# Optimization experiments

Hardware: AMD Instinct MI355X
Metric: run time of the kernel (lower is better)

The kernel has to match this reference:

```python
import jax, jax.numpy as jnp
import numpy as np

RBF_DIM = 64          # args.radius_emb_dim
FOLD_DIM = 128        # args.fold_dim
PROT_RADIUS = 30.0    # args.protein_radius (GaussianSmearing stop)
NP_, NL_, E_ = 100000, 50000, 500000


def gaussian_smearing(d):
    # GaussianSmearing(start=0, stop=PROT_RADIUS, num_gaussians=RBF_DIM)
    offsets = jnp.linspace(0.0, PROT_RADIUS, RBF_DIM, dtype=d.dtype)  # [R]
    coeff = -0.5 / (offsets[1] - offsets[0]) ** 2
    return jnp.exp(coeff * (d[:, None] - offsets[None, :]) ** 2)  # [E, R]


def setup_inputs() -> dict:
    key = jax.random.key(0)
    ks = jax.random.split(key, 12)
    scale = 10.0  # spread positions so distances span [0, PROT_RADIUS]
    pos = lambda k, n: jax.random.normal(k, (n, 3), jnp.float32) * scale
    inp = {
        'lig_pos': pos(ks[0], NL_),
        'prot_pos': pos(ks[1], NP_),
        'prot_pos_Cb': pos(ks[2], NP_),
        'prot_pos_C': pos(ks[3], NP_),
        'prot_pos_O': pos(ks[4], NP_),
        'prot_pos_N': pos(ks[5], NP_),
        'W1': jax.random.normal(ks[6], (5 * RBF_DIM, FOLD_DIM), jnp.float32) * 0.05,
        'b1': jnp.zeros((FOLD_DIM,), jnp.float32),
        'W2': jax.random.normal(ks[7], (FOLD_DIM, FOLD_DIM), jnp.float32) * 0.05,
        'b2': jnp.zeros((FOLD_DIM,), jnp.float32),
        'src': jax.random.randint(ks[8], (E_,), 0, NL_, jnp.int32),   # ligand index per edge
        'dst': jax.random.randint(ks[9], (E_,), 0, NP_, jnp.int32),   # protein index per edge
    }
    return inp


def reference(lig_pos, prot_pos, prot_pos_Cb, prot_pos_C, prot_pos_O, prot_pos_N,
              W1, b1, W2, b2, src, dst):
    lp = lig_pos[src]  # [E, 3] gather of ligand positions
    # 5 distance channels: CA/Cb/C/O/N protein atoms, each RBF-smeared
    feats = [gaussian_smearing(jnp.linalg.norm(lp - p[dst], axis=-1))
             for p in (prot_pos, prot_pos_Cb, prot_pos_C, prot_pos_O, prot_pos_N)]
    edge_attr = jnp.concatenate(feats, axis=-1)  # [E, 5*RBF_DIM]
    h = jax.nn.relu(edge_attr @ W1 + b1)         # [E, FOLD_DIM]
    return h @ W2 + b2                           # [E, FOLD_DIM]
```

## Files before the change

### kernel.cpp

```cpp
#include <hip/hip_runtime.h>
#include <hip/hip_bf16.h>

typedef unsigned short ushort_t;
typedef unsigned int uint_t;
typedef __attribute__((ext_vector_type(8))) short short8;
typedef __attribute__((ext_vector_type(4))) float f32x4;
typedef __attribute__((ext_vector_type(4))) uint_t uint4_t;
typedef __attribute__((ext_vector_type(2))) uint_t uint2_t;

#define FOLD 128
#define S_CONST 1.78357580f
#define DS_CONST 0.84932180f

__device__ __forceinline__ ushort_t f2bf(float f) {
    uint_t x = __builtin_bit_cast(uint_t, f);
    x += 0x7FFFu + ((x >> 16) & 1u);
    return (ushort_t)(x >> 16);
}

__device__ __forceinline__ uint_t pkbf(float a, float b) {
    uint_t xl = __builtin_bit_cast(uint_t, a);
    uint_t xh = __builtin_bit_cast(uint_t, b);
    uint_t rl = (xl + 0x7FFFu + ((xl >> 16) & 1u)) >> 16;
    uint_t rh = (xh + 0x7FFFu + ((xh >> 16) & 1u)) & 0xFFFF0000u;
    return rh | rl;
}

__global__ __launch_bounds__(256) void pack_w(const float* __restrict__ W1,
                                              const float* __restrict__ W2,
                                              ushort_t* __restrict__ W1p,
                                              ushort_t* __restrict__ W2p) {
    int i = blockIdx.x * 256 + threadIdx.x;
    if (i < 40960) {
        int j = i & 7, l = (i >> 3) & 63, nt = (i >> 9) & 7, ks = i >> 12;
        int row = ks * 32 + ((l >> 4) << 3) + j;
        int col = nt * 16 + (l & 15);
        W1p[i] = f2bf(W1[row * FOLD + col]);
    } else if (i < 40960 + 16384) {
        int q = i - 40960;
        int j = q & 7, l = (q >> 3) & 63, nt = (q >> 9) & 7, ks = q >> 12;
        int row = ks * 32 + ((l >> 4) << 3) + j;
        int col = nt * 16 + (l & 15);
        W2p[q] = f2bf(W2[row * FOLD + col]);
    }
}

#define TEDGE 64

__global__ __launch_bounds__(256, 2) void fused(
    const float* __restrict__ lig,
    const float* __restrict__ p0, const float* __restrict__ p1,
    const float* __restrict__ p2, const float* __restrict__ p3,
    const float* __restrict__ p4,
    const ushort_t* __restrict__ W1p, const ushort_t* __restrict__ W2p,
    const float* __restrict__ b1, const float* __restrict__ b2,
    const int* __restrict__ src, const int* __restrict__ dst,
    float* __restrict__ out, int E)
{
    __shared__ float d_lds[2][5][TEDGE];
    __shared__ alignas(16) uint_t attrU[TEDGE * 160];
    __shared__ alignas(16) uint_t h_u[TEDGE * 64];

    const int t = threadIdx.x;
    const int w = t >> 6;
    const int l = t & 63;
    const int lrow = l & 15, lgrp = l >> 4;
    const int aswz = (lrow & 7) << 2;
    const int ntiles = (E + TEDGE - 1) / TEDGE;

    const short8* W1v = reinterpret_cast<const short8*>(W1p);
    const short8* W2v = reinterpret_cast<const short8*>(W2p);
    short8 wb1[20], wb2[8];
    #pragma unroll
    for (int ks = 0; ks < 10; ++ks) {
        wb1[2 * ks]     = W1v[(ks * 8 + w * 2 + 0) * 64 + l];
        wb1[2 * ks + 1] = W1v[(ks * 8 + w * 2 + 1) * 64 + l];
    }
    #pragma unroll
    for (int ks = 0; ks < 4; ++ks) {
        wb2[2 * ks]     = W2v[(ks * 8 + w * 2 + 0) * 64 + l];
        wb2[2 * ks + 1] = W2v[(ks * 8 + w * 2 + 1) * 64 + l];
    }
    f32x4 hb1[2], hb2[2];
    hb1[0] = *reinterpret_cast<const f32x4*>(&b1[w * 32 + lgrp * 4]);
    hb1[1] = *reinterpret_cast<const f32x4*>(&b1[w * 32 + 16 + lgrp * 4]);
    hb2[0] = *reinterpret_cast<const f32x4*>(&b2[w * 32 + lgrp * 4]);
    hb2[1] = *reinterpret_cast<const f32x4*>(&b2[w * 32 + 16 + lgrp * 4]);

    const int g1c = t >> 6, g1m = t & 63;
    const bool gth2 = (t < 64);
    const float* GP1 = (g1c == 0) ? p0 : (g1c == 1) ? p1 : (g1c == 2) ? p2 : p3;
    const float* GP2 = p4;

    const int m2 = t >> 3, q2 = t & 7;
    const float ubase = (float)(8 * q2) * DS_CONST;

    int tile = blockIdx.x;
    if (tile >= ntiles) return;

    {
        int e = tile * TEDGE + g1m; if (e >= E) e = E - 1;
        int s = src[e], dd = dst[e];
        float dx = lig[3 * s]     - GP1[3 * dd];
        float dy = lig[3 * s + 1] - GP1[3 * dd + 1];
        float dz = lig[3 * s + 2] - GP1[3 * dd + 2];
        d_lds[0][g1c][g1m] = sqrtf(dx * dx + dy * dy + dz * dz);
        if (gth2) {
            float ex = lig[3 * s]     - GP2[3 * dd];
            float ey = lig[3 * s + 1] - GP2[3 * dd + 1];
            float ez = lig[3 * s + 2] - GP2[3 * dd + 2];
            d_lds[0][4][g1m] = sqrtf(ex * ex + ey * ey + ez * ez);
        }
    }
    __syncthreads();

    int buf = 0;
    while (true) {
        const int next = tile + gridDim.x;
        const bool havenext = (next < ntiles);

        float ax, ay, az, bx, by, bz, cx, cy, cz;
        if (havenext) {
            int e = next * TEDGE + g1m; if (e >= E) e = E - 1;
            int s = src[e], dd = dst[e];
            ax = lig[3 * s];     bx = GP1[3 * dd];
            ay = lig[3 * s + 1]; by = GP1[3 * dd + 1];
            az = lig[3 * s + 2]; bz = GP1[3 * dd + 2];
            if (gth2) {
                cx = GP2[3 * dd]; cy = GP2[3 * dd + 1]; cz = GP2[3 * dd + 2];
            }
        }

        #pragma unroll
        for (int half = 0; half < 2; ++half) {
            const int m = m2 + half * 32;
            const int swz = (m & 7) << 2;
            float dv[5];
            #pragma unroll
            for (int c = 0; c < 5; ++c) dv[c] = d_lds[buf][c][m];
            #pragma unroll
            for (int c = 0; c < 5; ++c) {
                float u0 = __builtin_fmaf(dv[c], S_CONST, -ubase);
                uint4_t vals;
                #pragma unroll
                for (int i = 0; i < 4; ++i) {
                    float ua = u0 - (float)(2 * i) * DS_CONST;
                    float ub = u0 - (float)(2 * i + 1) * DS_CONST;
                    float va = __builtin_amdgcn_exp2f(-(ua * ua));
                    float vb = __builtin_amdgcn_exp2f(-(ub * ub));
                    vals[i] = pkbf(va, vb);
                }
                int o = 32 * c + 4 * q2;
                *reinterpret_cast<uint4_t*>(&attrU[m * 160 + (o ^ swz)]) = vals;
            }
        }

        if (havenext) {
            float dx = ax - bx, dy = ay - by, dz = az - bz;
            d_lds[buf ^ 1][g1c][g1m] = sqrtf(dx * dx + dy * dy + dz * dz);
            if (gth2) {
                float ex = ax - cx, ey = ay - cy, ez = az - cz;
                d_lds[buf ^ 1][4][g1m] = sqrtf(ex * ex + ey * ey + ez * ez);
            }
        }
        __syncthreads();

        f32x4 g1[2][4];
        #pragma unroll
        for (int nh = 0; nh < 2; ++nh)
            #pragma unroll
            for (int eh = 0; eh < 4; ++eh) g1[nh][eh] = f32x4{0.f, 0.f, 0.f, 0.f};
        #pragma unroll
        for (int ks = 0; ks < 10; ++ks) {
            int o = ks * 16 + lgrp * 4;
            short8 af[4];
            #pragma unroll
            for (int eh = 0; eh < 4; ++eh)
                af[eh] = *reinterpret_cast<const short8*>(&attrU[(lrow + eh * 16) * 160 + (o ^ aswz)]);
            #pragma unroll
            for (int eh = 0; eh < 4; ++eh) {
                g1[0][eh] = __builtin_amdgcn_mfma_f32_16x16x32_bf16(wb1[2 * ks],     af[eh], g1[0][eh], 0, 0, 0);
                g1[1][eh] = __builtin_amdgcn_mfma_f32_16x16x32_bf16(wb1[2 * ks + 1], af[eh], g1[1][eh], 0, 0, 0);
            }
        }

        #pragma unroll
        for (int nh = 0; nh < 2; ++nh) {
            #pragma unroll
            for (int eh = 0; eh < 4; ++eh) {
                float v0 = fmaxf(g1[nh][eh][0] + hb1[nh][0], 0.f);
                float v1 = fmaxf(g1[nh][eh][1] + hb1[nh][1], 0.f);
                float v2 = fmaxf(g1[nh][eh][2] + hb1[nh][2], 0.f);
                float v3 = fmaxf(g1[nh][eh][3] + hb1[nh][3], 0.f);
                uint2_t pv;
                pv[0] = pkbf(v0, v1);
                pv[1] = pkbf(v2, v3);
                int e = eh * 16 + lrow;
                int dw = (w * 16 + nh * 8 + lgrp * 2) ^ ((e & 7) << 2);
                *reinterpret_cast<uint2_t*>(&h_u[e * 64 + dw]) = pv;
            }
        }
        __syncthreads();

        f32x4 o2[2][4];
        #pragma unroll
        for (int nh = 0; nh < 2; ++nh)
            #pragma unroll
            for (int eh = 0; eh < 4; ++eh) o2[nh][eh] = f32x4{0.f, 0.f, 0.f, 0.f};
        #pragma unroll
        for (int ks = 0; ks < 4; ++ks) {
            int dw = ks * 16 + lgrp * 4;
            short8 hf[4];
            #pragma unroll
            for (int eh = 0; eh < 4; ++eh)
                hf[eh] = *reinterpret_cast<const short8*>(&h_u[(lrow + eh * 16) * 64 + (dw ^ aswz)]);
            #pragma unroll
            for (int eh = 0; eh < 4; ++eh) {
                o2[0][eh] = __builtin_amdgcn_mfma_f32_16x16x32_bf16(wb2[2 * ks],     hf[eh], o2[0][eh], 0, 0, 0);
                o2[1][eh] = __builtin_amdgcn_mfma_f32_16x16x32_bf16(wb2[2 * ks + 1], hf[eh], o2[1][eh], 0, 0, 0);
            }
        }

        const int e0i = tile * TEDGE;
        #pragma unroll
        for (int nh = 0; nh < 2; ++nh) {
            #pragma unroll
            for (int eh = 0; eh < 4; ++eh) {
                int e = e0i + eh * 16 + lrow;
                if (e < E) {
                    f32x4 v = o2[nh][eh] + hb2[nh];
                    *reinterpret_cast<f32x4*>(&out[(size_t)e * FOLD + w * 32 + nh * 16 + lgrp * 4]) = v;
                }
            }
        }

        if (!havenext) break;
        tile = next;
        buf ^= 1;
    }
}

extern "C" void kernel_launch(void* const* d_in, const int* in_sizes, int n_in,
                              void* d_out, int out_size, void* d_ws, size_t ws_size,
                              hipStream_t stream) {
    const float* lig = (const float*)d_in[0];
    const float* p0  = (const float*)d_in[1];
    const float* p1  = (const float*)d_in[2];
    const float* p2  = (const float*)d_in[3];
    const float* p3  = (const float*)d_in[4];
    const float* p4  = (const float*)d_in[5];
    const float* W1  = (const float*)d_in[6];
    const float* b1  = (const float*)d_in[7];
    const float* W2  = (const float*)d_in[8];
    const float* b2  = (const float*)d_in[9];
    const int* src   = (const int*)d_in[10];
    const int* dst   = (const int*)d_in[11];
    float* out = (float*)d_out;
    const int E = in_sizes[10];

    ushort_t* W1p = (ushort_t*)d_ws;
    ushort_t* W2p = W1p + 40960;

    pack_w<<<(40960 + 16384 + 255) / 256, 256, 0, stream>>>(W1, W2, W1p, W2p);

    int tiles = (E + TEDGE - 1) / TEDGE;
    int nblk = tiles < 1024 ? tiles : 1024;
    fused<<<nblk, 256, 0, stream>>>(lig, p0, p1, p2, p3, p4, W1p, W2p,
                                    b1, b2, src, dst, out, E);
}
```

Measured before the change: 126.9 us.

## Prefetch edge indices two tiles ahead and use LDS-only barriers

Loads src/dst indices two tiles ahead, so the position gathers for the next tile no longer wait on a dependent index load. The next tile's distance computation and LDS write move to after the first GEMM, giving the gathered positions more time to arrive. Full __syncthreads are replaced by a barrier that waits only on LDS counters, so outstanding global loads can stay in flight across barriers. Output stores become nontemporal. This costs more live registers and relies on the custom barrier being correct for the LDS hazards.

```diff
diff --git a/kernel.cpp b/kernel.cpp
--- a/kernel.cpp
+++ b/kernel.cpp
@@ -24,6 +24,12 @@
     uint_t rl = (xl + 0x7FFFu + ((xl >> 16) & 1u)) >> 16;
     uint_t rh = (xh + 0x7FFFu + ((xh >> 16) & 1u)) & 0xFFFF0000u;
     return rh | rl;
+}
+
+__device__ __forceinline__ void softbar() {
+    asm volatile("s_waitcnt lgkmcnt(0)" ::: "memory");
+    __builtin_amdgcn_s_barrier();
+    asm volatile("" ::: "memory");
 }
 
 __global__ __launch_bounds__(256) void pack_w(const float* __restrict__ W1,
@@ -67,6 +73,7 @@
     const int lrow = l & 15, lgrp = l >> 4;
     const int aswz = (lrow & 7) << 2;
     const int ntiles = (E + TEDGE - 1) / TEDGE;
+    const int G = gridDim.x;
 
     const short8* W1v = reinterpret_cast<const short8*>(W1p);
     const short8* W2v = reinterpret_cast<const short8*>(W2p);
@@ -112,23 +119,29 @@
             d_lds[0][4][g1m] = sqrtf(ex * ex + ey * ey + ez * ez);
         }
     }
-    __syncthreads();
+    int sN = 0, dN = 0;
+    if (tile + G < ntiles) {
+        int e = (tile + G) * TEDGE + g1m; if (e >= E) e = E - 1;
+        sN = src[e]; dN = dst[e];
+    }
+    softbar();
 
     int buf = 0;
     while (true) {
-        const int next = tile + gridDim.x;
+        const int next = tile + G;
         const bool havenext = (next < ntiles);
 
         float ax, ay, az, bx, by, bz, cx, cy, cz;
         if (havenext) {
-            int e = next * TEDGE + g1m; if (e >= E) e = E - 1;
-            int s = src[e], dd = dst[e];
-            ax = lig[3 * s];     bx = GP1[3 * dd];
-            ay = lig[3 * s + 1]; by = GP1[3 * dd + 1];
-            az = lig[3 * s + 2]; bz = GP1[3 * dd + 2];
-            if (gth2) {
-                cx = GP2[3 * dd]; cy = GP2[3 * dd + 1]; cz = GP2[3 * dd + 2];
-            }
+            ax = lig[3 * sN];     bx = GP1[3 * dN];
+            ay = lig[3 * sN + 1]; by = GP1[3 * dN + 1];
+            az = lig[3 * sN + 2]; bz = GP1[3 * dN + 2];
+            if (gth2) { cx = GP2[3 * dN]; cy = GP2[3 * dN + 1]; cz = GP2[3 * dN + 2]; }
+        }
+        int sN2 = sN, dN2 = dN;
+        if (next + G < ntiles) {
+            int e = (next + G) * TEDGE + g1m; if (e >= E) e = E - 1;
+            sN2 = src[e]; dN2 = dst[e];
         }
 
         #pragma unroll
@@ -154,16 +167,7 @@
                 *reinterpret_cast<uint4_t*>(&attrU[m * 160 + (o ^ swz)]) = vals;
             }
         }
-
-        if (havenext) {
-            float dx = ax - bx, dy = ay - by, dz = az - bz;
-            d_lds[buf ^ 1][g1c][g1m] = sqrtf(dx * dx + dy * dy + dz * dz);
-            if (gth2) {
-                float ex = ax - cx, ey = ay - cy, ez = az - cz;
-                d_lds[buf ^ 1][4][g1m] = sqrtf(ex * ex + ey * ey + ez * ez);
-            }
-        }
-        __syncthreads();
+        softbar();
 
         f32x4 g1[2][4];
         #pragma unroll
@@ -200,7 +204,17 @@
                 *reinterpret_cast<uint2_t*>(&h_u[e * 64 + dw]) = pv;
             }
         }
-        __syncthreads();
+
+        if (havenext) {
+            float dx = ax - bx, dy = ay - by, dz = az - bz;
+            d_lds[buf ^ 1][g1c][g1m] = sqrtf(dx * dx + dy * dy + dz * dz);
+            if (gth2) {
+                float ex = ax - cx, ey = ay - cy, ez = az - cz;
+                d_lds[buf ^ 1][4][g1m] = sqrtf(ex * ex + ey * ey + ez * ez);
+            }
+        }
+        sN = sN2; dN = dN2;
+        softbar();
 
         f32x4 o2[2][4];
         #pragma unroll
@@ -229,7 +243,8 @@
                 int e = e0i + eh * 16 + lrow;
                 if (e < E) {
                     f32x4 v = o2[nh][eh] + hb2[nh];
-                    *reinterpret_cast<f32x4*>(&out[(size_t)e * FOLD + w * 32 + nh * 16 + lgrp * 4]) = v;
+                    __builtin_nontemporal_store(v,
+                        reinterpret_cast<f32x4*>(&out[(size_t)e * FOLD + w * 32 + nh * 16 + lgrp * 4]));
                 }
             }
         }
```

Result: faster. 115.3 us (-9.2%).
